# Optimization experiments

Measured on AMD Instinct MI355X. Metric: run time of the kernel, lower is better.

Reference implementation:

```python
import jax, jax.numpy as jnp
import numpy as np

N, E, IN, H0, H1 = 50000, 1600000, 64, 64, 128


def _gcn(h, W, b, row, col):
    # PyG GCNConv, add_self_loops=False, unit edge weights:
    # out[col] += d^{-1/2}[row] * d^{-1/2}[col] * (h @ W)[row]; bias added after aggregation
    n = h.shape[0]
    deg = jnp.zeros((n,), h.dtype).at[col].add(jnp.ones((row.shape[0],), h.dtype))
    dinv = jnp.where(deg > 0, jax.lax.rsqrt(jnp.maximum(deg, 1e-12)), 0.0)
    norm = (dinv[row] * dinv[col])[:, None]  # [E,1]
    m = h @ W  # transform before propagate (small GEMM)
    out = jnp.zeros((n, W.shape[1]), h.dtype).at[col].add(norm * m[row])
    return out + b


def _bn(h, g, b):
    # BatchNorm1d training-mode math (biased variance), eps=1e-5
    mu = h.mean(0)
    var = ((h - mu) ** 2).mean(0)
    return g * (h - mu) * jax.lax.rsqrt(var + 1e-5) + b


def _san(h):
    return jnp.nan_to_num(h, nan=0.0, posinf=100.0, neginf=-100.0)


def _slice(x, ei, W0, b0, W1, b1, res1, g0, be0, g1, be1):
    row, col = ei[0], ei[1]
    # layer 0: conv -> bn -> relu -> (dropout=eval identity) -> residual (Identity, 64==64) -> nan_to_num
    h1 = _san(jax.nn.relu(_bn(_gcn(x, W0, b0, row, col), g0, be0)) + x)
    # layer 1 (last): conv -> bn -> residual (Linear proj 64->128, no bias) -> nan_to_num
    h2 = _san(_bn(_gcn(h1, W1, b1, row, col), g1, be1) + h1 @ res1)
    return h2


def setup_inputs() -> dict:
    k = jax.random.split(jax.random.key(0), 16)
    f = lambda kk, sh, s: jax.random.normal(kk, sh, jnp.float32) * s
    return {
        "x": f(k[0], (N, IN), 1.0),
        "edge_index0": jax.random.randint(k[1], (2, E), 0, N),
        "edge_index1": jax.random.randint(k[2], (2, E), 0, N),
        "w0_s0": f(k[3], (IN, H0), 0.1), "b0_s0": jnp.zeros((H0,), jnp.float32),
        "w1_s0": f(k[4], (H0, H1), 0.1), "b1_s0": jnp.zeros((H1,), jnp.float32),
        "res1_s0": f(k[5], (H0, H1), 0.1),
        "w0_s1": f(k[6], (IN, H0), 0.1), "b0_s1": jnp.zeros((H0,), jnp.float32),
        "w1_s1": f(k[7], (H0, H1), 0.1), "b1_s1": jnp.zeros((H1,), jnp.float32),
        "res1_s1": f(k[8], (H0, H1), 0.1),
        "bn_g0": jnp.ones((H0,), jnp.float32), "bn_b0": jnp.zeros((H0,), jnp.float32),
        "bn_g1": jnp.ones((H1,), jnp.float32), "bn_b1": jnp.zeros((H1,), jnp.float32),
        "fc1_w": f(k[9], (2 * H1, H1), 0.1), "fc1_b": jnp.zeros((H1,), jnp.float32),
        "fc2_w": f(k[10], (H1, 2), 0.1), "fc2_b": jnp.zeros((2,), jnp.float32),
    }


def reference(x, edge_index0, edge_index1,
              w0_s0, b0_s0, w1_s0, b1_s0, res1_s0,
              w0_s1, b0_s1, w1_s1, b1_s1, res1_s1,
              bn_g0, bn_b0, bn_g1, bn_b1,
              fc1_w, fc1_b, fc2_w, fc2_b):
    out0 = _slice(x, edge_index0, w0_s0, b0_s0, w1_s0, b1_s0, res1_s0, bn_g0, bn_b0, bn_g1, bn_b1)
    out1 = _slice(x, edge_index1, w0_s1, b0_s1, w1_s1, b1_s1, res1_s1, bn_g0, bn_b0, bn_g1, bn_b1)
    combined = jnp.concatenate([out0, out1], axis=1)  # [N, 2*H1]
    h = jax.nn.relu(combined @ fc1_w + fc1_b)  # dropout is eval-mode identity
    logits = h @ fc2_w + fc2_b
    return logits, jax.nn.softmax(logits, axis=1)
```

## Files before the change

kernel.cpp:

```cpp
#include <hip/hip_runtime.h>
#include <hip/hip_bf16.h>
#include <math.h>


typedef short v8s __attribute__((ext_vector_type(8)));
typedef float f32x4 __attribute__((ext_vector_type(4)));

#define BSTRIDE 10240

__device__ __forceinline__ float sanf(float v) {
    if (v != v) return 0.f;
    if (isinf(v)) return v > 0.f ? 100.f : -100.f;
    return v;
}

__device__ __forceinline__ unsigned short bf16of(float v) {
    __hip_bfloat16 h = __float2bfloat16(v);
    return *(unsigned short*)&h;
}
__device__ __forceinline__ unsigned pack2(float lo, float hi) {
    return (unsigned)bf16of(lo) | ((unsigned)bf16of(hi) << 16);
}
__device__ __forceinline__ float uflo(unsigned u) { return __uint_as_float(u << 16); }
__device__ __forceinline__ float ufhi(unsigned u) { return __uint_as_float(u & 0xFFFF0000u); }
__device__ __forceinline__ float fofbf16(unsigned short u) {
    return __uint_as_float(((unsigned)u) << 16);
}

__device__ __forceinline__ void packone(const float* __restrict__ src, unsigned* __restrict__ dst,
                                        int L, int Khalf, int F) {
    int c = L / Khalf, kp = L - c * Khalf;
    dst[L] = pack2(src[(2 * kp) * F + c], src[(2 * kp + 1) * F + c]);
}

__global__ __launch_bounds__(256) void prep_kernel(const float* __restrict__ w0_0,
                                                   const float* __restrict__ w0_1,
                                                   const float* __restrict__ w1_0,
                                                   const float* __restrict__ w1_1,
                                                   const float* __restrict__ r_0,
                                                   const float* __restrict__ r_1,
                                                   const float* __restrict__ fc1,
                                                   unsigned* __restrict__ wpk,
                                                   int* __restrict__ bcnt,
                                                   float* __restrict__ sums) {
    int gid = blockIdx.x * 256 + threadIdx.x;
    if (gid < 512) bcnt[gid] = 0;
    if (gid < 8192) sums[gid] = 0.f;
    if (gid < 2048)       packone(w0_0, wpk + 0,     gid - 0,     32, 64);
    else if (gid < 4096)  packone(w0_1, wpk + 2048,  gid - 2048,  32, 64);
    else if (gid < 8192)  packone(w1_0, wpk + 4096,  gid - 4096,  32, 128);
    else if (gid < 12288) packone(w1_1, wpk + 8192,  gid - 8192,  32, 128);
    else if (gid < 16384) packone(r_0,  wpk + 12288, gid - 12288, 32, 128);
    else if (gid < 20480) packone(r_1,  wpk + 16384, gid - 16384, 32, 128);
    else if (gid < 36864) packone(fc1,  wpk + 20480, gid - 20480, 128, 128);
}


__global__ __launch_bounds__(512) void kC_bin(const int* __restrict__ ei0,
                                              const int* __restrict__ ei1,
                                              int* __restrict__ bcnt,
                                              unsigned* __restrict__ binned,
                                              int E, int n) {
    __shared__ int cnt[512];
    __shared__ int base[512];
    int t = threadIdx.x;
    cnt[t] = 0;
    int E2 = 2 * E;
    int e0 = blockIdx.x * 8192;
    unsigned pk[16];
    int bk[16];
    __syncthreads();
#pragma unroll
    for (int j = 0; j < 16; ++j) {
        int ge = e0 + t + j * 512;
        bk[j] = -1;
        if (ge < E2) {
            int slice = ge >= E;
            const int* ei = slice ? ei1 : ei0;
            int e = ge - slice * E;
            int col = ei[E + e], row = ei[e];
            int gcol = slice * n + col;
            bk[j] = gcol >> 8;
            pk[j] = (unsigned)row | (((unsigned)gcol & 255u) << 16);
            atomicAdd(&cnt[bk[j]], 1);
        }
    }
    __syncthreads();
    {
        int c = cnt[t];
        base[t] = c ? atomicAdd(&bcnt[t], c) : 0;
    }
    __syncthreads();
    cnt[t] = 0;
    __syncthreads();
#pragma unroll
    for (int j = 0; j < 16; ++j) {
        if (bk[j] >= 0) {
            int loc = atomicAdd(&cnt[bk[j]], 1);
            int off = base[bk[j]] + loc;
            if (off < BSTRIDE) binned[(size_t)bk[j] * BSTRIDE + off] = pk[j];
        }
    }
}

__global__ __launch_bounds__(256) void kB_scan(const int* __restrict__ bcnt,
                                               int* __restrict__ bstart, int NB) {
    __shared__ int tmp[256];
    int t = threadIdx.x, carry = 0;
    for (int bse = 0; bse < NB; bse += 256) {
        int i = bse + t;
        int v = (i < NB) ? bcnt[i] : 0;
        tmp[t] = v;
        __syncthreads();
        for (int off = 1; off < 256; off <<= 1) {
            int u = (t >= off) ? tmp[t - off] : 0;
            __syncthreads();
            tmp[t] += u;
            __syncthreads();
        }
        if (i < NB) bstart[i] = tmp[t] - v + carry;
        carry += tmp[255];
        __syncthreads();
    }
    if (t == 0) bstart[NB] = carry;
}

__global__ __launch_bounds__(512) void kD_build(const unsigned* __restrict__ binned,
                                                const int* __restrict__ bstart,
                                                int* __restrict__ rowptr,
                                                float* __restrict__ dinv,
                                                unsigned short* __restrict__ csr,
                                                int n2, int NB) {
    __shared__ int cnt[256];
    __shared__ int scn[256];
    __shared__ int cur[256];
    int b = blockIdx.x, t = threadIdx.x;
    int s = bstart[b], e = bstart[b + 1];
    int m = e - s;
    const unsigned* seg = binned + (size_t)b * BSTRIDE;
    if (t < 256) cnt[t] = 0;
    __syncthreads();
    for (int i = t; i < m; i += 512) atomicAdd(&cnt[(seg[i] >> 16) & 255], 1);
    __syncthreads();
    int v = (t < 256) ? cnt[t] : 0;
    if (t < 256) scn[t] = v;
    __syncthreads();
    for (int off = 1; off < 256; off <<= 1) {
        int u = (t < 256 && t >= off) ? scn[t - off] : 0;
        __syncthreads();
        if (t < 256) scn[t] += u;
        __syncthreads();
    }
    if (t < 256) {
        int excl = scn[t] - v;
        int gcol = b * 256 + t;
        if (gcol < n2) {
            rowptr[gcol] = s + excl;
            dinv[gcol] = v > 0 ? rsqrtf((float)v) : 0.f;
        }
        cur[t] = excl;
    }
    __syncthreads();
    for (int i = t; i < m; i += 512) {
        unsigned p = seg[i];
        int cl = (p >> 16) & 255;
        int pos = s + atomicAdd(&cur[cl], 1);
        csr[pos] = (unsigned short)(p & 0xFFFFu);
    }
    if (b == 0 && t == 0) rowptr[n2] = bstart[NB];
}


__global__ __launch_bounds__(256) void prescale_bf(const float* __restrict__ x,
                                                   const float* __restrict__ dinv,
                                                   unsigned short* __restrict__ xsb,
                                                   int n64, int n) {
    int i = blockIdx.x * 256 + threadIdx.x;
    if (i >= n64) return;
    int row = i >> 6;
    float v = x[i];
    xsb[i] = bf16of(v * dinv[row]);
    xsb[n64 + i] = bf16of(v * dinv[n + row]);
}

__global__ __launch_bounds__(256) void gatherbf_kernel(const int* __restrict__ rowptr,
                                                       const unsigned short* __restrict__ csr,
                                                       const unsigned short* __restrict__ m,
                                                       const float* __restrict__ dinv,
                                                       unsigned short* __restrict__ outb,
                                                       int n, int n2) {
    int gid = blockIdx.x * 256 + threadIdx.x;
    int node = gid >> 3;
    if (node >= n2) return;
    int l = threadIdx.x & 7;
    const unsigned short* mb = m + (size_t)((node >= n) ? n : 0) * 64;
    int s = rowptr[node], e = rowptr[node + 1];
    float a0 = 0.f, a1 = 0.f, a2 = 0.f, a3 = 0.f, a4 = 0.f, a5 = 0.f, a6 = 0.f, a7 = 0.f;
    int b = s;
    for (; b + 8 <= e; b += 8) {
        int idx = csr[b + l];
        uint4 u[8];
#pragma unroll
        for (int j = 0; j < 8; ++j) {
            int r = __shfl(idx, j, 8);
            u[j] = *(const uint4*)&mb[(size_t)r * 64 + l * 8];
        }
#pragma unroll
        for (int j = 0; j < 8; ++j) {
            a0 += uflo(u[j].x); a1 += ufhi(u[j].x);
            a2 += uflo(u[j].y); a3 += ufhi(u[j].y);
            a4 += uflo(u[j].z); a5 += ufhi(u[j].z);
            a6 += uflo(u[j].w); a7 += ufhi(u[j].w);
        }
    }
    if (b < e) {
        int cntn = e - b;
        int idx = (b + l < e) ? (int)csr[b + l] : 0;
        for (int j = 0; j < cntn; ++j) {
            int r = __shfl(idx, j, 8);
            uint4 u = *(const uint4*)&mb[(size_t)r * 64 + l * 8];
            a0 += uflo(u.x); a1 += ufhi(u.x);
            a2 += uflo(u.y); a3 += ufhi(u.y);
            a4 += uflo(u.z); a5 += ufhi(u.z);
            a6 += uflo(u.w); a7 += ufhi(u.w);
        }
    }
    float d = dinv[node];
    uint4 o;
    o.x = pack2(a0 * d, a1 * d);
    o.y = pack2(a2 * d, a3 * d);
    o.z = pack2(a4 * d, a5 * d);
    o.w = pack2(a6 * d, a7 * d);
    *(uint4*)&outb[(size_t)node * 64 + l * 8] = o;
}


template <int F>
__global__ __launch_bounds__(256) void mfma_gemmb(const unsigned short* __restrict__ Ab,
                                                  const unsigned* __restrict__ WT0,
                                                  const unsigned* __restrict__ WT1,
                                                  unsigned short* __restrict__ Cb,
                                                  float* __restrict__ sums_base,
                                                  int roff, int n) {
    constexpr int NC = F / 16;
    __shared__ float ls[2 * F];
    int BPS = (n + 63) >> 6;
    int slice = blockIdx.x >= BPS;
    int sb = blockIdx.x - slice * BPS;
    const unsigned* WT = slice ? WT1 : WT0;
    int row0 = slice * n + sb * 64;
    int rows = min(64, n - sb * 64);
    for (int i = threadIdx.x; i < 2 * F; i += 256) ls[i] = 0.f;
    int w = threadIdx.x >> 6, lane = threadIdx.x & 63, q = lane >> 4, ln = lane & 15;
    const unsigned* A32 = (const unsigned*)Ab;
    size_t arow = (size_t)(row0 + 16 * w + ln) * 32;
    v8s af0 = *(const v8s*)&A32[arow + q * 4];
    v8s af1 = *(const v8s*)&A32[arow + 16 + q * 4];
    f32x4 acc[NC];
#pragma unroll
    for (int ct = 0; ct < NC; ++ct) acc[ct] = {0.f, 0.f, 0.f, 0.f};
#pragma unroll
    for (int ct = 0; ct < NC; ++ct) {
        v8s b0 = *(const v8s*)&WT[(ct * 16 + ln) * 32 + q * 4];
        v8s b1 = *(const v8s*)&WT[(ct * 16 + ln) * 32 + 16 + q * 4];
        acc[ct] = __builtin_amdgcn_mfma_f32_16x16x32_bf16(af0, b0, acc[ct], 0, 0, 0);
        acc[ct] = __builtin_amdgcn_mfma_f32_16x16x32_bf16(af1, b1, acc[ct], 0, 0, 0);
    }
    __syncthreads();
#pragma unroll
    for (int ct = 0; ct < NC; ++ct) {
        float s1 = 0.f, s2 = 0.f;
#pragma unroll
        for (int i = 0; i < 4; ++i) {
            int r = 16 * w + q * 4 + i;
            if (r < rows) {
                float v = acc[ct][i];
                Cb[(size_t)(row0 + r) * F + ct * 16 + ln] = bf16of(v);
                s1 += v;
                s2 += v * v;
            }
        }
        s1 += __shfl_xor(s1, 16); s1 += __shfl_xor(s1, 32);
        s2 += __shfl_xor(s2, 16); s2 += __shfl_xor(s2, 32);
        if (q == 0) {
            atomicAdd(&ls[ct * 16 + ln], s1);
            atomicAdd(&ls[F + ct * 16 + ln], s2);
        }
    }
    __syncthreads();
    if (threadIdx.x < F) {
        float* dst = sums_base + (blockIdx.x & 7) * 1024 + roff + slice * 2 * F;
        unsafeAtomicAdd(&dst[threadIdx.x], ls[threadIdx.x]);
        unsafeAtomicAdd(&dst[F + threadIdx.x], ls[F + threadIdx.x]);
    }
}

__global__ __launch_bounds__(256) void mfma_apply1(const unsigned short* __restrict__ h1b,
                                                   const unsigned short* __restrict__ Tb,
                                                   const unsigned* __restrict__ RT0,
                                                   const unsigned* __restrict__ RT1,
                                                   const float* __restrict__ scsh,
                                                   unsigned short* __restrict__ comb, int n) {
    int BPS = (n + 63) >> 6;
    int slice = blockIdx.x >= BPS;
    int sb = blockIdx.x - slice * BPS;
    const unsigned* WT = slice ? RT1 : RT0;
    int row0 = slice * n + sb * 64;
    int rows = min(64, n - sb * 64);
    int w = threadIdx.x >> 6, lane = threadIdx.x & 63, q = lane >> 4, ln = lane & 15;
    const unsigned* A32 = (const unsigned*)h1b;
    size_t arow = (size_t)(row0 + 16 * w + ln) * 32;
    v8s af0 = *(const v8s*)&A32[arow + q * 4];
    v8s af1 = *(const v8s*)&A32[arow + 16 + q * 4];
    f32x4 acc[8];
#pragma unroll
    for (int ct = 0; ct < 8; ++ct) acc[ct] = {0.f, 0.f, 0.f, 0.f};
#pragma unroll
    for (int ct = 0; ct < 8; ++ct) {
        v8s b0 = *(const v8s*)&WT[(ct * 16 + ln) * 32 + q * 4];
        v8s b1 = *(const v8s*)&WT[(ct * 16 + ln) * 32 + 16 + q * 4];
        acc[ct] = __builtin_amdgcn_mfma_f32_16x16x32_bf16(af0, b0, acc[ct], 0, 0, 0);
        acc[ct] = __builtin_amdgcn_mfma_f32_16x16x32_bf16(af1, b1, acc[ct], 0, 0, 0);
    }
    const float* sc = scsh + slice * 256;
#pragma unroll
    for (int ct = 0; ct < 8; ++ct) {
        int c = ct * 16 + ln;
        float scale = sc[c], shift = sc[128 + c];
#pragma unroll
        for (int i = 0; i < 4; ++i) {
            int r = 16 * w + q * 4 + i;
            if (r >= rows) continue;
            int row = row0 + r;
            float tv = fofbf16(Tb[(size_t)row * 128 + c]);
            float o = sanf(fmaf(tv, scale, shift) + acc[ct][i]);
            comb[(size_t)(row - slice * n) * 256 + slice * 128 + c] = bf16of(o);
        }
    }
}

__global__ __launch_bounds__(256) void mfma_head_fc2(const unsigned short* __restrict__ comb,
                                                     const unsigned* __restrict__ FT,
                                                     const float* __restrict__ bias,
                                                     const float* __restrict__ w2,
                                                     const float* __restrict__ b2,
                                                     float* __restrict__ out, int n) {
    int row0 = blockIdx.x * 64;
    int rows = min(64, n - row0);
    int w = threadIdx.x >> 6, lane = threadIdx.x & 63, q = lane >> 4, ln = lane & 15;
    const unsigned* A32 = (const unsigned*)comb;
    size_t arow = (size_t)(row0 + 16 * w + ln) * 128;
    f32x4 acc[8];
#pragma unroll
    for (int ct = 0; ct < 8; ++ct) acc[ct] = {0.f, 0.f, 0.f, 0.f};
#pragma unroll
    for (int kt = 0; kt < 4; ++kt) {
        v8s af0 = *(const v8s*)&A32[arow + kt * 32 + q * 4];
        v8s af1 = *(const v8s*)&A32[arow + kt * 32 + 16 + q * 4];
#pragma unroll
        for (int ct = 0; ct < 8; ++ct) {
            v8s b0 = *(const v8s*)&FT[(ct * 16 + ln) * 128 + kt * 32 + q * 4];
            v8s b1 = *(const v8s*)&FT[(ct * 16 + ln) * 128 + kt * 32 + 16 + q * 4];
            acc[ct] = __builtin_amdgcn_mfma_f32_16x16x32_bf16(af0, b0, acc[ct], 0, 0, 0);
            acc[ct] = __builtin_amdgcn_mfma_f32_16x16x32_bf16(af1, b1, acc[ct], 0, 0, 0);
        }
    }
    float p0[4] = {0.f, 0.f, 0.f, 0.f}, p1[4] = {0.f, 0.f, 0.f, 0.f};
#pragma unroll
    for (int ct = 0; ct < 8; ++ct) {
        int c = ct * 16 + ln;
        float bi = bias[c];
        float w20 = w2[c * 2], w21 = w2[c * 2 + 1];
#pragma unroll
        for (int i = 0; i < 4; ++i) {
            float h = fmaxf(acc[ct][i] + bi, 0.f);
            p0[i] = fmaf(h, w20, p0[i]);
            p1[i] = fmaf(h, w21, p1[i]);
        }
    }
#pragma unroll
    for (int i = 0; i < 4; ++i) {
#pragma unroll
        for (int msk = 1; msk < 16; msk <<= 1) {
            p0[i] += __shfl_xor(p0[i], msk);
            p1[i] += __shfl_xor(p1[i], msk);
        }
    }
    if (ln == 0) {
        float bb0 = b2[0], bb1 = b2[1];
#pragma unroll
        for (int i = 0; i < 4; ++i) {
            int r = 16 * w + q * 4 + i;
            if (r >= rows) continue;
            int R = row0 + r;
            float l0 = p0[i] + bb0, l1 = p1[i] + bb1;
            float mx = fmaxf(l0, l1);
            float e0 = expf(l0 - mx), e1 = expf(l1 - mx);
            float inv = 1.0f / (e0 + e1);
            out[(size_t)R * 2] = l0;
            out[(size_t)R * 2 + 1] = l1;
            out[(size_t)2 * n + R * 2] = e0 * inv;
            out[(size_t)2 * n + R * 2 + 1] = e1 * inv;
        }
    }
}


template <int F>
__global__ void bnfinal_kernel(const float* __restrict__ sums_base, int roff,
                               const float* __restrict__ g,
                               const float* __restrict__ be, float* __restrict__ scsh, int n) {
    int f = threadIdx.x;
    if (f >= F) return;
    int slice = blockIdx.x;
    float s1 = 0.f, s2 = 0.f;
#pragma unroll
    for (int r = 0; r < 8; ++r) {
        const float* src = sums_base + r * 1024 + roff + slice * 2 * F;
        s1 += src[f];
        s2 += src[F + f];
    }
    float inv_n = 1.0f / (float)n;
    float mu = s1 * inv_n;
    float var = fmaxf(s2 * inv_n - mu * mu, 0.f);
    float scale = g[f] * rsqrtf(var + 1e-5f);
    scsh[slice * 2 * F + f] = scale;
    scsh[slice * 2 * F + F + f] = be[f] - mu * scale;
}

__global__ __launch_bounds__(256) void apply0_kernel(const unsigned short* __restrict__ t0b,
                                                     const float* __restrict__ x,
                                                     const float* __restrict__ scsh,
                                                     const float* __restrict__ dinv,
                                                     unsigned short* __restrict__ h1b,
                                                     unsigned short* __restrict__ h1sb,
                                                     int n64, int total) {
    int i = blockIdx.x * 256 + threadIdx.x;
    if (i >= total) return;
    int slice = i >= n64;
    int f = i & 63;
    const float* sc = scsh + slice * 128;
    float v = fmaf(fofbf16(t0b[i]), sc[f], sc[64 + f]);
    v = fmaxf(v, 0.f) + x[i - slice * n64];
    v = sanf(v);
    h1b[i] = bf16of(v);
    h1sb[i] = bf16of(v * dinv[i >> 6]);
}

static inline int cdiv(int a, int b) { return (a + b - 1) / b; }

extern "C" void kernel_launch(void* const* d_in, const int* in_sizes, int n_in,
                              void* d_out, int out_size, void* d_ws, size_t ws_size,
                              hipStream_t stream) {
    const float* x       = (const float*)d_in[0];
    const int*   ei0     = (const int*)d_in[1];
    const int*   ei1     = (const int*)d_in[2];
    const float* w0_s0   = (const float*)d_in[3];
    const float* w1_s0   = (const float*)d_in[5];
    const float* res1_s0 = (const float*)d_in[7];
    const float* w0_s1   = (const float*)d_in[8];
    const float* w1_s1   = (const float*)d_in[10];
    const float* res1_s1 = (const float*)d_in[12];
    const float* bn_g0   = (const float*)d_in[13];
    const float* bn_b0   = (const float*)d_in[14];
    const float* bn_g1   = (const float*)d_in[15];
    const float* bn_b1   = (const float*)d_in[16];
    const float* fc1_w   = (const float*)d_in[17];
    const float* fc1_b   = (const float*)d_in[18];
    const float* fc2_w   = (const float*)d_in[19];
    const float* fc2_b   = (const float*)d_in[20];
    float* out = (float*)d_out;

    int n = in_sizes[0] / 64;
    int E = in_sizes[1] / 2;
    int n2 = 2 * n, E2 = 2 * E;
    int n64 = n * 64;
    int NB = cdiv(n2, 256);
    int BPS = cdiv(n, 64);

    float* X1 = (float*)d_ws;
    float* S  = X1 + (size_t)n2 * 64;
    unsigned short* Gb   = (unsigned short*)(S + (size_t)n2 * 64);
    unsigned short* h1b  = Gb + (size_t)n2 * 64;
    unsigned short* comb = h1b + (size_t)n2 * 64;
    unsigned short* xsb  = comb + (size_t)n * 256;
    float* dinv = (float*)(xsb + (size_t)n * 128);
    float* sums = dinv + n2;
    float* scsh = sums + 8192;
    unsigned* wpk = (unsigned*)(scsh + 512);
    unsigned short* csr = (unsigned short*)(wpk + 36864);
    int* rowptr = (int*)(csr + (size_t)E2);
    int* bcnt   = rowptr + (n2 + 1);
    int* bstart = bcnt + 512;
    unsigned short* t0b = (unsigned short*)X1;
    unsigned short* Tb  = (unsigned short*)X1;
    unsigned* binned = (unsigned*)comb;
    unsigned short* h1sb = (unsigned short*)S;
    unsigned* w0T0 = wpk + 0,    *w0T1 = wpk + 2048;
    unsigned* w1T0 = wpk + 4096, *w1T1 = wpk + 8192;
    unsigned* rT0  = wpk + 12288,*rT1  = wpk + 16384;
    unsigned* fT   = wpk + 20480;

    prep_kernel<<<144, 256, 0, stream>>>(w0_s0, w0_s1, w1_s0, w1_s1,
                                         res1_s0, res1_s1, fc1_w, wpk, bcnt, sums);
    kC_bin<<<cdiv(E2, 8192), 512, 0, stream>>>(ei0, ei1, bcnt, binned, E, n);
    kB_scan<<<1, 256, 0, stream>>>(bcnt, bstart, NB);
    kD_build<<<NB, 512, 0, stream>>>(binned, bstart, rowptr, dinv, csr, n2, NB);

    prescale_bf<<<cdiv(n64, 256), 256, 0, stream>>>(x, dinv, xsb, n64, n);
    gatherbf_kernel<<<cdiv(n2 * 8, 256), 256, 0, stream>>>(rowptr, csr, xsb, dinv, Gb, n, n2);
    mfma_gemmb<64><<<2 * BPS, 256, 0, stream>>>(Gb, w0T0, w0T1, t0b, sums, 512, n);
    bnfinal_kernel<64><<<2, 64, 0, stream>>>(sums, 512, bn_g0, bn_b0, scsh, n);
    apply0_kernel<<<cdiv(2 * n64, 256), 256, 0, stream>>>(t0b, x, scsh, dinv, h1b, h1sb, n64, 2 * n64);

    gatherbf_kernel<<<cdiv(n2 * 8, 256), 256, 0, stream>>>(rowptr, csr, h1sb, dinv, Gb, n, n2);
    mfma_gemmb<128><<<2 * BPS, 256, 0, stream>>>(Gb, w1T0, w1T1, Tb, sums, 0, n);
    bnfinal_kernel<128><<<2, 128, 0, stream>>>(sums, 0, bn_g1, bn_b1, scsh, n);
    mfma_apply1<<<2 * BPS, 256, 0, stream>>>(h1b, Tb, rT0, rT1, scsh, comb, n);

    mfma_head_fc2<<<BPS, 256, 0, stream>>>(comb, fT, fc1_b, fc2_w, fc2_b, out, n);
}
```

Measured before the change: 383.3 us.

## Vectorize elementwise kernels and stage MFMA outputs through LDS for coalesced stores

Prescale and apply0 now handle 8 elements per thread, using float4 and uint4 loads and stores in place of scalar accesses. The gemm and apply1 epilogues write MFMA accumulators into swizzled shared memory, then each thread writes out contiguous 16-byte chunks of a row. This replaces 2-byte strided global stores and scalar reads of Tb with coalesced vector accesses. The cost is more shared memory per block, which may reduce occupancy: 32KB for apply1 and up to 16KB for the gemm.

After: 372.5 us. -2.8%, faster.

```diff
diff --git a/kernel.cpp b/kernel.cpp
--- a/kernel.cpp
+++ b/kernel.cpp
@@ -175,12 +175,19 @@
                                                    const float* __restrict__ dinv,
                                                    unsigned short* __restrict__ xsb,
                                                    int n64, int n) {
-    int i = blockIdx.x * 256 + threadIdx.x;
-    if (i >= n64) return;
-    int row = i >> 6;
-    float v = x[i];
-    xsb[i] = bf16of(v * dinv[row]);
-    xsb[n64 + i] = bf16of(v * dinv[n + row]);
+    int i8 = (blockIdx.x * 256 + threadIdx.x) * 8;
+    if (i8 >= n64) return;
+    int row = i8 >> 6;
+    float4 v0 = *(const float4*)&x[i8];
+    float4 v1 = *(const float4*)&x[i8 + 4];
+    float d0 = dinv[row], d1 = dinv[n + row];
+    uint4 o0, o1;
+    o0.x = pack2(v0.x * d0, v0.y * d0); o0.y = pack2(v0.z * d0, v0.w * d0);
+    o0.z = pack2(v1.x * d0, v1.y * d0); o0.w = pack2(v1.z * d0, v1.w * d0);
+    o1.x = pack2(v0.x * d1, v0.y * d1); o1.y = pack2(v0.z * d1, v0.w * d1);
+    o1.z = pack2(v1.x * d1, v1.y * d1); o1.w = pack2(v1.z * d1, v1.w * d1);
+    *(uint4*)&xsb[i8] = o0;
+    *(uint4*)&xsb[n64 + i8] = o1;
 }
 
 __global__ __launch_bounds__(256) void gatherbf_kernel(const int* __restrict__ rowptr,
@@ -244,6 +251,7 @@
                                                   int roff, int n) {
     constexpr int NC = F / 16;
     __shared__ float ls[2 * F];
+    __shared__ unsigned short stb[64 * F];
     int BPS = (n + 63) >> 6;
     int slice = blockIdx.x >= BPS;
     int sb = blockIdx.x - slice * BPS;
@@ -270,12 +278,13 @@
 #pragma unroll
     for (int ct = 0; ct < NC; ++ct) {
         float s1 = 0.f, s2 = 0.f;
+        int cc = ct * 16 + ln;
 #pragma unroll
         for (int i = 0; i < 4; ++i) {
             int r = 16 * w + q * 4 + i;
+            stb[r * F + (cc ^ ((r & 7) << 3))] = bf16of(acc[ct][i]);
             if (r < rows) {
                 float v = acc[ct][i];
-                Cb[(size_t)(row0 + r) * F + ct * 16 + ln] = bf16of(v);
                 s1 += v;
                 s2 += v * v;
             }
@@ -283,11 +292,23 @@
         s1 += __shfl_xor(s1, 16); s1 += __shfl_xor(s1, 32);
         s2 += __shfl_xor(s2, 16); s2 += __shfl_xor(s2, 32);
         if (q == 0) {
-            atomicAdd(&ls[ct * 16 + ln], s1);
-            atomicAdd(&ls[F + ct * 16 + ln], s2);
-        }
-    }
-    __syncthreads();
+            atomicAdd(&ls[cc], s1);
+            atomicAdd(&ls[F + cc], s2);
+        }
+    }
+    __syncthreads();
+    {
+        constexpr int CPT = F / 4;
+        int rr = threadIdx.x >> 2, sg = threadIdx.x & 3;
+        if (rr < rows) {
+            int swz = (rr & 7) << 3;
+            int cb = sg * CPT;
+            uint4* dst = (uint4*)(Cb + (size_t)(row0 + rr) * F + cb);
+#pragma unroll
+            for (int jj = 0; jj < CPT / 8; ++jj)
+                dst[jj] = *(const uint4*)&stb[rr * F + ((cb + jj * 8) ^ swz)];
+        }
+    }
     if (threadIdx.x < F) {
         float* dst = sums_base + (blockIdx.x & 7) * 1024 + roff + slice * 2 * F;
         unsafeAtomicAdd(&dst[threadIdx.x], ls[threadIdx.x]);
@@ -301,6 +322,7 @@
                                                    const unsigned* __restrict__ RT1,
                                                    const float* __restrict__ scsh,
                                                    unsigned short* __restrict__ comb, int n) {
+    __shared__ float st[64 * 128];
     int BPS = (n + 63) >> 6;
     int slice = blockIdx.x >= BPS;
     int sb = blockIdx.x - slice * BPS;
@@ -322,20 +344,47 @@
         acc[ct] = __builtin_amdgcn_mfma_f32_16x16x32_bf16(af0, b0, acc[ct], 0, 0, 0);
         acc[ct] = __builtin_amdgcn_mfma_f32_16x16x32_bf16(af1, b1, acc[ct], 0, 0, 0);
     }
-    const float* sc = scsh + slice * 256;
 #pragma unroll
     for (int ct = 0; ct < 8; ++ct) {
-        int c = ct * 16 + ln;
-        float scale = sc[c], shift = sc[128 + c];
+        int cc = ct * 16 + ln;
 #pragma unroll
         for (int i = 0; i < 4; ++i) {
             int r = 16 * w + q * 4 + i;
-            if (r >= rows) continue;
-            int row = row0 + r;
-            float tv = fofbf16(Tb[(size_t)row * 128 + c]);
-            float o = sanf(fmaf(tv, scale, shift) + acc[ct][i]);
-            comb[(size_t)(row - slice * n) * 256 + slice * 128 + c] = bf16of(o);
-        }
+            st[r * 128 + (cc ^ ((r & 7) << 2))] = acc[ct][i];
+        }
+    }
+    __syncthreads();
+    int rr = threadIdx.x >> 2, sg = threadIdx.x & 3;
+    if (rr >= rows) return;
+    int swz = (rr & 7) << 2;
+    int rg = row0 + rr;
+    const uint4* tbp = (const uint4*)(Tb + (size_t)rg * 128 + sg * 32);
+    const float* scb = scsh + slice * 256 + sg * 32;
+    uint4* outp = (uint4*)(comb + (size_t)(rg - slice * n) * 256 + slice * 128 + sg * 32);
+#pragma unroll
+    for (int jj = 0; jj < 4; ++jj) {
+        uint4 t = tbp[jj];
+        int base = sg * 32 + jj * 8;
+        float4 a0 = *(const float4*)&st[rr * 128 + (base ^ swz)];
+        float4 a1 = *(const float4*)&st[rr * 128 + ((base + 4) ^ swz)];
+        float4 s0 = *(const float4*)&scb[jj * 8];
+        float4 s1 = *(const float4*)&scb[jj * 8 + 4];
+        float4 h0 = *(const float4*)&scb[128 + jj * 8];
+        float4 h1v = *(const float4*)&scb[128 + jj * 8 + 4];
+        float o0 = sanf(fmaf(uflo(t.x), s0.x, h0.x) + a0.x);
+        float o1 = sanf(fmaf(ufhi(t.x), s0.y, h0.y) + a0.y);
+        float o2 = sanf(fmaf(uflo(t.y), s0.z, h0.z) + a0.z);
+        float o3 = sanf(fmaf(ufhi(t.y), s0.w, h0.w) + a0.w);
+        float o4 = sanf(fmaf(uflo(t.z), s1.x, h1v.x) + a1.x);
+        float o5 = sanf(fmaf(ufhi(t.z), s1.y, h1v.y) + a1.y);
+        float o6 = sanf(fmaf(uflo(t.w), s1.z, h1v.z) + a1.z);
+        float o7 = sanf(fmaf(ufhi(t.w), s1.w, h1v.w) + a1.w);
+        uint4 ov;
+        ov.x = pack2(o0, o1);
+        ov.y = pack2(o2, o3);
+        ov.z = pack2(o4, o5);
+        ov.w = pack2(o6, o7);
+        outp[jj] = ov;
     }
 }
 
@@ -435,16 +484,35 @@
                                                      unsigned short* __restrict__ h1b,
                                                      unsigned short* __restrict__ h1sb,
                                                      int n64, int total) {
-    int i = blockIdx.x * 256 + threadIdx.x;
-    if (i >= total) return;
-    int slice = i >= n64;
-    int f = i & 63;
+    int i8 = (blockIdx.x * 256 + threadIdx.x) * 8;
+    if (i8 >= total) return;
+    int slice = i8 >= n64;
+    int f0 = i8 & 63;
     const float* sc = scsh + slice * 128;
-    float v = fmaf(fofbf16(t0b[i]), sc[f], sc[64 + f]);
-    v = fmaxf(v, 0.f) + x[i - slice * n64];
-    v = sanf(v);
-    h1b[i] = bf16of(v);
-    h1sb[i] = bf16of(v * dinv[i >> 6]);
+    uint4 t = *(const uint4*)&t0b[i8];
+    const float* xp = x + (i8 - slice * n64);
+    float4 x0 = *(const float4*)xp;
+    float4 x1 = *(const float4*)(xp + 4);
+    float4 s0 = *(const float4*)&sc[f0];
+    float4 s1 = *(const float4*)&sc[f0 + 4];
+    float4 g0 = *(const float4*)&sc[64 + f0];
+    float4 g1 = *(const float4*)&sc[64 + f0 + 4];
+    float d = dinv[i8 >> 6];
+    float tv[8] = {uflo(t.x), ufhi(t.x), uflo(t.y), ufhi(t.y),
+                   uflo(t.z), ufhi(t.z), uflo(t.w), ufhi(t.w)};
+    float sa[8] = {s0.x, s0.y, s0.z, s0.w, s1.x, s1.y, s1.z, s1.w};
+    float sh[8] = {g0.x, g0.y, g0.z, g0.w, g1.x, g1.y, g1.z, g1.w};
+    float xv[8] = {x0.x, x0.y, x0.z, x0.w, x1.x, x1.y, x1.z, x1.w};
+    unsigned po[4], ps[4];
+#pragma unroll
+    for (int j = 0; j < 4; ++j) {
+        float a = sanf(fmaxf(fmaf(tv[2 * j], sa[2 * j], sh[2 * j]), 0.f) + xv[2 * j]);
+        float b = sanf(fmaxf(fmaf(tv[2 * j + 1], sa[2 * j + 1], sh[2 * j + 1]), 0.f) + xv[2 * j + 1]);
+        po[j] = pack2(a, b);
+        ps[j] = pack2(a * d, b * d);
+    }
+    *(uint4*)&h1b[i8] = *(uint4*)po;
+    *(uint4*)&h1sb[i8] = *(uint4*)ps;
 }
 
 static inline int cdiv(int a, int b) { return (a + b - 1) / b; }
@@ -507,11 +575,11 @@
     kB_scan<<<1, 256, 0, stream>>>(bcnt, bstart, NB);
     kD_build<<<NB, 512, 0, stream>>>(binned, bstart, rowptr, dinv, csr, n2, NB);
 
-    prescale_bf<<<cdiv(n64, 256), 256, 0, stream>>>(x, dinv, xsb, n64, n);
+    prescale_bf<<<cdiv(n64, 2048), 256, 0, stream>>>(x, dinv, xsb, n64, n);
     gatherbf_kernel<<<cdiv(n2 * 8, 256), 256, 0, stream>>>(rowptr, csr, xsb, dinv, Gb, n, n2);
     mfma_gemmb<64><<<2 * BPS, 256, 0, stream>>>(Gb, w0T0, w0T1, t0b, sums, 512, n);
     bnfinal_kernel<64><<<2, 64, 0, stream>>>(sums, 512, bn_g0, bn_b0, scsh, n);
-    apply0_kernel<<<cdiv(2 * n64, 256), 256, 0, stream>>>(t0b, x, scsh, dinv, h1b, h1sb, n64, 2 * n64);
+    apply0_kernel<<<cdiv(2 * n64, 2048), 256, 0, stream>>>(t0b, x, scsh, dinv, h1b, h1sb, n64, 2 * n64);
 
     gatherbf_kernel<<<cdiv(n2 * 8, 256), 256, 0, stream>>>(rowptr, csr, h1sb, dinv, Gb, n, n2);
     mfma_gemmb<128><<<2 * BPS, 256, 0, stream>>>(Gb, w1T0, w1T1, Tb, sums, 0, n);
```
